# Kernel tuning notes

Measured on AMD Instinct MI355X. Metric: run time of the kernel, lower is better.

The kernel has to match this reference:

```python
import jax, jax.numpy as jnp
import numpy as np

ALPHA = 16
M_FACTORS = [8, 16, 8]
N_FACTORS = [8, 16, 8]


def setup_inputs() -> dict:
    key = jax.random.key(0)
    ks = jax.random.split(key, 9)
    B, S, D = 8, 2048, 1024
    r = 8
    x = jax.random.normal(ks[0], (B, S, D), dtype=jnp.float32)
    W = jax.random.normal(ks[1], (D, D), dtype=jnp.float32) * 0.02
    b = jax.random.normal(ks[2], (D,), dtype=jnp.float32) * 0.02
    # m-cores: (r_prev, m_i, r_next), first rank = 1
    core0 = jax.random.normal(ks[3], (1, 8, r), dtype=jnp.float32) * 0.1
    core1 = jax.random.normal(ks[4], (r, 16, r), dtype=jnp.float32) * 0.1
    core2 = jax.random.normal(ks[5], (r, 8, r), dtype=jnp.float32) * 0.1
    # n-cores: (r_prev, n_i, r_next), last rank = 1
    core3 = jax.random.normal(ks[6], (r, 8, r), dtype=jnp.float32) * 0.1
    core4 = jax.random.normal(ks[7], (r, 16, r), dtype=jnp.float32) * 0.1
    core5 = jax.random.normal(ks[8], (r, 8, 1), dtype=jnp.float32) * 0.1
    return {"x": x, "W": W, "b": b, "core0": core0, "core1": core1,
            "core2": core2, "core3": core3, "core4": core4, "core5": core5}


def tensorized_multiplication(x, m_cores, n_cores, m_factors):
    B, S, _ = x.shape
    # [B, 1, S, m_k, ..., m_1] : input dim split into m_factors, reversed
    tt = x.reshape((B, S) + tuple(m_factors[::-1]))[:, None]
    for core in m_cores:
        # contract trailing m-factor and current rank, new rank at axis 1
        tt = jnp.einsum('br...m,rmp->bp...', tt, core)
    for core in n_cores:
        # expand n-factor at the end, carry rank at axis 1
        tt = jnp.einsum('br...,rnp->bp...n', tt, core)
    # tt: [B, 1, S, n_1, ..., n_k] -> [B, S, prod(n_factors)]
    return tt.reshape(B, S, -1)


def reference(x, W, b, core0, core1, core2, core3, core4, core5):
    z = tensorized_multiplication(x, [core0, core1, core2],
                                  [core3, core4, core5], M_FACTORS)
    base = jnp.einsum('bsd,od->bso', x, W) + b  # nn.Linear: x @ W.T + b
    return base + z * ALPHA
```

## Files before the change

kernel.cpp:

```cpp
#include <hip/hip_runtime.h>
#include <hip/hip_bf16.h>


#define D_DIM 1024
#define BS_ROWS 16384
#define ALPHA_F 16.0f
#define BM 128
#define BN 128

using bf16   = __bf16;
using bf16x8 = __attribute__((ext_vector_type(8))) __bf16;
using bf16x4 = __attribute__((ext_vector_type(4))) __bf16;
using f32x4  = __attribute__((ext_vector_type(4))) float;
using f32x16 = __attribute__((ext_vector_type(16))) float;

#define GPTR(p) (const __attribute__((address_space(1))) void*)(p)
#define SPTR(p) (__attribute__((address_space(3))) void*)(p)

__global__ __launch_bounds__(256) void make_mn_kernel(
    const float* __restrict__ c0, const float* __restrict__ c1,
    const float* __restrict__ c2, const float* __restrict__ c3,
    const float* __restrict__ c4, const float* __restrict__ c5,
    float* __restrict__ Mws, float* __restrict__ NTws)
{
    __shared__ float sh[128 * 9];
    const int tid = threadIdx.x;

    if (blockIdx.x < 32) {
        for (int e = tid; e < 1024; e += 256) {
            int p2 = e & 7, i2i1 = e >> 3;
            int i1 = i2i1 & 7, i2 = i2i1 >> 3;
            float s = 0.f;
            for (int p1 = 0; p1 < 8; ++p1)
                s += c0[i1 * 8 + p1] * c1[p1 * 128 + i2 * 8 + p2];
            sh[i2i1 * 9 + p2] = s;
        }
        __syncthreads();
        int e = blockIdx.x * 256 + tid;
        int p3 = e & 7, d = e >> 3;
        int i1 = d & 7, i2 = (d >> 3) & 15, i3 = d >> 7;
        float s = 0.f;
        for (int p2 = 0; p2 < 8; ++p2)
            s += sh[(i2 * 8 + i1) * 9 + p2] * c2[p2 * 64 + i3 * 8 + p3];
        Mws[e] = s;
    } else {
        for (int e = tid; e < 1024; e += 256) {
            int p4 = e & 7, nn = e >> 3;
            int n2 = nn >> 3, n3 = nn & 7;
            float s = 0.f;
            for (int p5 = 0; p5 < 8; ++p5)
                s += c4[p4 * 128 + n2 * 8 + p5] * c5[p5 * 8 + n3];
            sh[nn * 9 + p4] = s;
        }
        __syncthreads();
        int e = (blockIdx.x - 32) * 256 + tid;
        int r3 = e & 7, o = e >> 3;
        int n1 = o >> 7, nn = o & 127;
        float s = 0.f;
        for (int p4 = 0; p4 < 8; ++p4)
            s += c3[r3 * 64 + n1 * 8 + p4] * sh[nn * 9 + p4];
        NTws[o * 8 + r3] = s;
    }
}

__global__ __launch_bounds__(256) void weff_cast_kernel(
    const float* __restrict__ X, const float* __restrict__ W,
    const float* __restrict__ Mws, const float* __restrict__ NTws,
    bf16* __restrict__ Weff, bf16* __restrict__ Xb)
{
    const int tid = threadIdx.x;
    if (blockIdx.x >= 512) {
        size_t i = ((size_t)(blockIdx.x - 512) * 256 + tid) * 8;
        f32x4 a = *(const f32x4*)&X[i];
        f32x4 b = *(const f32x4*)&X[i + 4];
        bf16x8 v;
        v[0] = (bf16)a[0]; v[1] = (bf16)a[1]; v[2] = (bf16)a[2]; v[3] = (bf16)a[3];
        v[4] = (bf16)b[0]; v[5] = (bf16)b[1]; v[6] = (bf16)b[2]; v[7] = (bf16)b[3];
        *(bf16x8*)&Xb[i] = v;
        return;
    }
    int e  = blockIdx.x * 256 + tid;
    int o  = e >> 7;
    int d0 = (e & 127) * 8;
    f32x4 nt0 = *(const f32x4*)&NTws[o * 8];
    f32x4 nt1 = *(const f32x4*)&NTws[o * 8 + 4];
    f32x4 w0 = *(const f32x4*)&W[(size_t)o * D_DIM + d0];
    f32x4 w1 = *(const f32x4*)&W[(size_t)o * D_DIM + d0 + 4];
    bf16x8 res;
    for (int k = 0; k < 8; ++k) {
        f32x4 m0 = *(const f32x4*)&Mws[(d0 + k) * 8];
        f32x4 m1 = *(const f32x4*)&Mws[(d0 + k) * 8 + 4];
        float acc = m0[0]*nt0[0] + m0[1]*nt0[1] + m0[2]*nt0[2] + m0[3]*nt0[3]
                  + m1[0]*nt1[0] + m1[1]*nt1[1] + m1[2]*nt1[2] + m1[3]*nt1[3];
        float w = (k < 4) ? w0[k] : w1[k - 4];
        res[k] = (bf16)(w + ALPHA_F * acc);
    }
    *(bf16x8*)&Weff[(size_t)o * D_DIM + d0] = res;
}

#define TBM 256
#define TBN 256
#define TBK 64
#define ABYT (TBM * TBK * 2)
#define BBYT (TBN * TBK * 2)
#define BUF4 (ABYT + BBYT)
#define NT4  (D_DIM / TBK)

__global__ __launch_bounds__(512, 2) void gemm_pipe4_kernel(
    const bf16* __restrict__ Xb,
    const bf16* __restrict__ Weff,
    const float* __restrict__ bias,
    float* __restrict__ Out)
{
    extern __shared__ __attribute__((aligned(16))) char smem[];

    const int tid  = threadIdx.x;
    const int wave = tid >> 6, lane = tid & 63;

    const int bid   = blockIdx.x;
    const int slot  = (bid & 7) * 32 + (bid >> 3);
    const int mtile = slot >> 2;
    const int ntile = slot & 3;

    const int wr = wave >> 2, wc = wave & 3;
    const int l31 = lane & 31, half = lane >> 5;
    const int rsw = l31 & 7;

    const int srow   = wave * 32 + (lane >> 3);
    const int gchunk = (lane & 7) ^ (lane >> 3);
    const bf16* asrc = Xb   + (size_t)(mtile * TBM + srow) * D_DIM + gchunk * 8;
    const bf16* bsrc = Weff + (size_t)(ntile * TBN + srow) * D_DIM + gchunk * 8;
    const int woff = wave * 4096;

    auto STAGE = [&](int bo, int t) {
        const bf16* ap = asrc + t * TBK;
        const bf16* bp = bsrc + t * TBK;
#pragma unroll
        for (int j = 0; j < 4; ++j)
            __builtin_amdgcn_global_load_lds(GPTR(ap + (size_t)j * 8 * D_DIM),
                                             SPTR(smem + bo + woff + j * 1024), 16, 0, 0);
#pragma unroll
        for (int j = 0; j < 4; ++j)
            __builtin_amdgcn_global_load_lds(GPTR(bp + (size_t)j * 8 * D_DIM),
                                             SPTR(smem + bo + ABYT + woff + j * 1024), 16, 0, 0);
    };

    f32x16 acc[4][2];
#pragma unroll
    for (int i = 0; i < 4; ++i)
#pragma unroll
        for (int j = 0; j < 2; ++j)
#pragma unroll
            for (int r = 0; r < 16; ++r) acc[i][j][r] = 0.f;

    auto COMPUTE = [&](int bo) {
        const char* Ab = smem + bo;
        const char* Bb = smem + bo + ABYT;
#pragma unroll
        for (int kk = 0; kk < 4; ++kk) {
            const int sb = (((kk * 2 + half) ^ rsw) * 16);
            bf16x8 af[4], bfr[2];
#pragma unroll
            for (int i = 0; i < 4; ++i)
                af[i] = *(const bf16x8*)(Ab + (wr * 128 + i * 32 + l31) * 128 + sb);
#pragma unroll
            for (int j = 0; j < 2; ++j)
                bfr[j] = *(const bf16x8*)(Bb + (wc * 64 + j * 32 + l31) * 128 + sb);
            __builtin_amdgcn_s_setprio(1);
#pragma unroll
            for (int i = 0; i < 4; ++i)
#pragma unroll
                for (int j = 0; j < 2; ++j)
                    acc[i][j] = __builtin_amdgcn_mfma_f32_32x32x16_bf16(
                        af[i], bfr[j], acc[i][j], 0, 0, 0);
            __builtin_amdgcn_s_setprio(0);
        }
    };

    STAGE(0, 0);
    STAGE(BUF4, 1);
    asm volatile("s_waitcnt vmcnt(8)" ::: "memory");
    __builtin_amdgcn_s_barrier();
    __builtin_amdgcn_sched_barrier(0);

    for (int t = 0; t < NT4 - 2; ++t) {
        const int bo = (t & 1) * BUF4;
        COMPUTE(bo);
        asm volatile("s_waitcnt lgkmcnt(0)" ::: "memory");
        __builtin_amdgcn_s_barrier();
        __builtin_amdgcn_sched_barrier(0);
        STAGE(bo, t + 2);
        asm volatile("s_waitcnt vmcnt(8)" ::: "memory");
        __builtin_amdgcn_s_barrier();
        __builtin_amdgcn_sched_barrier(0);
    }
    COMPUTE(((NT4 - 2) & 1) * BUF4);
    asm volatile("s_waitcnt lgkmcnt(0)" ::: "memory");
    __builtin_amdgcn_s_barrier();
    __builtin_amdgcn_sched_barrier(0);
    asm volatile("s_waitcnt vmcnt(0)" ::: "memory");
    __builtin_amdgcn_s_barrier();
    __builtin_amdgcn_sched_barrier(0);
    COMPUTE(((NT4 - 1) & 1) * BUF4);

    float bj[2];
#pragma unroll
    for (int j = 0; j < 2; ++j)
        bj[j] = bias[ntile * TBN + wc * 64 + j * 32 + l31];
#pragma unroll
    for (int i = 0; i < 4; ++i) {
        int rbase = mtile * TBM + wr * 128 + i * 32 + 4 * half;
#pragma unroll
        for (int j = 0; j < 2; ++j) {
            int col = ntile * TBN + wc * 64 + j * 32 + l31;
#pragma unroll
            for (int r = 0; r < 16; ++r) {
                int row = rbase + (r & 3) + 8 * (r >> 2);
                Out[(size_t)row * D_DIM + col] = acc[i][j][r] + bj[j];
            }
        }
    }
}

__global__ __launch_bounds__(256) void gemm_bb_kernel(
    const bf16* __restrict__ Xb,
    const bf16* __restrict__ Weff,
    const float* __restrict__ bias,
    float* __restrict__ Out)
{
    __shared__ __align__(16) bf16 As[BM][64];
    __shared__ __align__(16) bf16 Bs[BN][64];

    const int tid  = threadIdx.x;
    const int wave = tid >> 6, lane = tid & 63;
    const int mtile = blockIdx.x, ntile = blockIdx.y;
    const int wr = wave >> 1, wc = wave & 1;
    const int l15 = lane & 15, quad = lane >> 4;

    const int srow = wave * 32 + (lane >> 3);
    const int gchunk = (lane & 7) ^ (lane >> 3);
    const bf16* asrc = Xb   + (size_t)(mtile * BM + srow) * D_DIM + gchunk * 8;
    const bf16* bsrc = Weff + (size_t)(ntile * BN + srow) * D_DIM + gchunk * 8;
    char* abase = (char*)&As[0][0] + wave * 4096;
    char* bbase = (char*)&Bs[0][0] + wave * 4096;

    const int rsw = l15 & 7;

    f32x4 acc[4][4];
    for (int i = 0; i < 4; ++i)
        for (int j = 0; j < 4; ++j)
            for (int r = 0; r < 4; ++r) acc[i][j][r] = 0.f;

    for (int kt = 0; kt < D_DIM / 64; ++kt) {
        const int ko = kt * 64;
        for (int j = 0; j < 4; ++j) {
            __builtin_amdgcn_global_load_lds(GPTR(asrc + (size_t)j * 8 * D_DIM + ko),
                                             SPTR(abase + j * 1024), 16, 0, 0);
            __builtin_amdgcn_global_load_lds(GPTR(bsrc + (size_t)j * 8 * D_DIM + ko),
                                             SPTR(bbase + j * 1024), 16, 0, 0);
        }
        __syncthreads();
        for (int kk = 0; kk < 2; ++kk) {
            const int lc = kk * 4 + quad;
            const int sc = (lc ^ rsw) * 8;
            bf16x8 af[4], bfr[4];
            for (int i = 0; i < 4; ++i)
                af[i] = *(const bf16x8*)&As[wr * 64 + i * 16 + l15][sc];
            for (int j = 0; j < 4; ++j)
                bfr[j] = *(const bf16x8*)&Bs[wc * 64 + j * 16 + l15][sc];
            for (int i = 0; i < 4; ++i)
                for (int j = 0; j < 4; ++j)
                    acc[i][j] = __builtin_amdgcn_mfma_f32_16x16x32_bf16(
                        af[i], bfr[j], acc[i][j], 0, 0, 0);
        }
        __syncthreads();
    }

    float bj[4];
    for (int j = 0; j < 4; ++j)
        bj[j] = bias[ntile * BN + wc * 64 + j * 16 + l15];
    for (int i = 0; i < 4; ++i) {
        int row0 = mtile * BM + wr * 64 + i * 16 + quad * 4;
        for (int r = 0; r < 4; ++r) {
            float* orow = Out + (size_t)(row0 + r) * D_DIM + ntile * BN + wc * 64 + l15;
            for (int j = 0; j < 4; ++j)
                orow[j * 16] = acc[i][j][r] + bj[j];
        }
    }
}

__global__ __launch_bounds__(256) void gemm_bias_kernel(
    const float* __restrict__ X,
    const bf16* __restrict__ Weff,
    const float* __restrict__ bias,
    float* __restrict__ Out)
{
    __shared__ __align__(16) bf16 As[BM][32];
    __shared__ __align__(16) bf16 Bs[BN][32];

    const int tid  = threadIdx.x;
    const int wave = tid >> 6, lane = tid & 63;
    const int mtile = blockIdx.x, ntile = blockIdx.y;
    const int wr = wave >> 1, wc = wave & 1;
    const int l15 = lane & 15, quad = lane >> 4;

    const int ar = tid >> 1, ah = tid & 1;
    const float* xsrc = X + (size_t)(mtile * BM + ar) * D_DIM + ah * 16;
    bf16* adst = &As[ar][ah * 16];

    const bf16* bsrc0 = Weff + (size_t)(ntile * BN + wave * 32 + (lane >> 2)) * D_DIM
                        + (lane & 3) * 8;
    const bf16* bsrc1 = bsrc0 + 16 * D_DIM;
    char* bbase = (char*)&Bs[0][0];
    void* bdst0 = bbase + wave * 2048;
    void* bdst1 = bbase + wave * 2048 + 1024;

    f32x4 acc[4][4];
    for (int i = 0; i < 4; ++i)
        for (int j = 0; j < 4; ++j)
            for (int r = 0; r < 4; ++r) acc[i][j][r] = 0.f;

    for (int kt = 0; kt < D_DIM / 32; ++kt) {
        __builtin_amdgcn_global_load_lds(GPTR(bsrc0 + kt * 32), SPTR(bdst0), 16, 0, 0);
        __builtin_amdgcn_global_load_lds(GPTR(bsrc1 + kt * 32), SPTR(bdst1), 16, 0, 0);

        const f32x4* xp = (const f32x4*)(xsrc + kt * 32);
        f32x4 f0 = xp[0], f1 = xp[1], f2 = xp[2], f3 = xp[3];
        bf16x8 p0, p1;
        p0[0] = (bf16)f0[0]; p0[1] = (bf16)f0[1]; p0[2] = (bf16)f0[2]; p0[3] = (bf16)f0[3];
        p0[4] = (bf16)f1[0]; p0[5] = (bf16)f1[1]; p0[6] = (bf16)f1[2]; p0[7] = (bf16)f1[3];
        p1[0] = (bf16)f2[0]; p1[1] = (bf16)f2[1]; p1[2] = (bf16)f2[2]; p1[3] = (bf16)f2[3];
        p1[4] = (bf16)f3[0]; p1[5] = (bf16)f3[1]; p1[6] = (bf16)f3[2]; p1[7] = (bf16)f3[3];
        *(bf16x8*)adst = p0;
        *(bf16x8*)(adst + 8) = p1;

        __syncthreads();

        bf16x8 af[4], bfr[4];
        for (int i = 0; i < 4; ++i)
            af[i] = *(const bf16x8*)&As[wr * 64 + i * 16 + l15][quad * 8];
        for (int j = 0; j < 4; ++j)
            bfr[j] = *(const bf16x8*)&Bs[wc * 64 + j * 16 + l15][quad * 8];
        for (int i = 0; i < 4; ++i)
            for (int j = 0; j < 4; ++j)
                acc[i][j] = __builtin_amdgcn_mfma_f32_16x16x32_bf16(
                    af[i], bfr[j], acc[i][j], 0, 0, 0);

        __syncthreads();
    }

    float bj[4];
    for (int j = 0; j < 4; ++j)
        bj[j] = bias[ntile * BN + wc * 64 + j * 16 + l15];
    for (int i = 0; i < 4; ++i) {
        int row0 = mtile * BM + wr * 64 + i * 16 + quad * 4;
        for (int r = 0; r < 4; ++r) {
            float* orow = Out + (size_t)(row0 + r) * D_DIM + ntile * BN + wc * 64 + l15;
            for (int j = 0; j < 4; ++j)
                orow[j * 16] = acc[i][j][r] + bj[j];
        }
    }
}

__global__ __launch_bounds__(256) void build_weff_fused_kernel(
    const float* __restrict__ W,
    const float* __restrict__ c0, const float* __restrict__ c1,
    const float* __restrict__ c2, const float* __restrict__ c3,
    const float* __restrict__ c4, const float* __restrict__ c5,
    bf16* __restrict__ Weff)
{
    __shared__ float t2[1024];
    __shared__ float Msh[8192];
    const int tid = threadIdx.x;
    const int o = blockIdx.x;

    for (int e = tid; e < 1024; e += 256) {
        int p2 = e & 7, i2i1 = e >> 3;
        int i1 = i2i1 & 7, i2 = i2i1 >> 3;
        float s = 0.f;
        for (int p1 = 0; p1 < 8; ++p1)
            s += c0[i1 * 8 + p1] * c1[p1 * 128 + i2 * 8 + p2];
        t2[e] = s;
    }
    __syncthreads();
    for (int e = tid; e < 8192; e += 256) {
        int p3 = e & 7, d = e >> 3;
        int i1 = d & 7, i2 = (d >> 3) & 15, i3 = d >> 7;
        float s = 0.f;
        for (int p2 = 0; p2 < 8; ++p2)
            s += t2[(i2 * 8 + i1) * 8 + p2] * c2[p2 * 64 + i3 * 8 + p3];
        Msh[e] = s;
    }
    int n1 = o >> 7, nn = o & 127, n2 = nn >> 3, n3 = nn & 7;
    float v[8];
    for (int p4 = 0; p4 < 8; ++p4) {
        float s = 0.f;
        for (int p5 = 0; p5 < 8; ++p5)
            s += c4[p4 * 128 + n2 * 8 + p5] * c5[p5 * 8 + n3];
        v[p4] = s;
    }
    float ncol[8];
    for (int r3 = 0; r3 < 8; ++r3) {
        float s = 0.f;
        for (int p4 = 0; p4 < 8; ++p4)
            s += c3[r3 * 64 + n1 * 8 + p4] * v[p4];
        ncol[r3] = s;
    }
    __syncthreads();

    int d0 = tid * 4;
    f32x4 w = *(const f32x4*)&W[o * D_DIM + d0];
    bf16x4 res;
    for (int k = 0; k < 4; ++k) {
        float acc = 0.f;
        for (int r = 0; r < 8; ++r)
            acc += Msh[(d0 + k) * 8 + r] * ncol[r];
        res[k] = (bf16)(w[k] + ALPHA_F * acc);
    }
    *(bf16x4*)&Weff[o * D_DIM + d0] = res;
}

extern "C" void kernel_launch(void* const* d_in, const int* in_sizes, int n_in,
                              void* d_out, int out_size, void* d_ws, size_t ws_size,
                              hipStream_t stream) {
    const float* x  = (const float*)d_in[0];
    const float* W  = (const float*)d_in[1];
    const float* b  = (const float*)d_in[2];
    const float* c0 = (const float*)d_in[3];
    const float* c1 = (const float*)d_in[4];
    const float* c2 = (const float*)d_in[5];
    const float* c3 = (const float*)d_in[6];
    const float* c4 = (const float*)d_in[7];
    const float* c5 = (const float*)d_in[8];
    float* out = (float*)d_out;

    char* ws = (char*)d_ws;
    bf16*  Weff = (bf16*)ws;
    float* Mws  = (float*)(ws + 2u * 1024u * 1024u);
    float* NTws = Mws + 8192;
    bf16*  Xb   = (bf16*)(ws + 4u * 1024u * 1024u);
    const size_t need = 4u * 1024u * 1024u + (size_t)BS_ROWS * D_DIM * 2u;

    static int smem_ok = -1;
    if (smem_ok < 0) {
        hipError_t e = hipFuncSetAttribute((const void*)gemm_pipe4_kernel,
                                           hipFuncAttributeMaxDynamicSharedMemorySize,
                                           2 * BUF4);
        smem_ok = (e == hipSuccess) ? 1 : 0;
    }

    if (ws_size >= need) {
        make_mn_kernel<<<64, 256, 0, stream>>>(c0, c1, c2, c3, c4, c5, Mws, NTws);
        weff_cast_kernel<<<512 + 8192, 256, 0, stream>>>(x, W, Mws, NTws, Weff, Xb);
        if (smem_ok) {
            gemm_pipe4_kernel<<<dim3(256), 512, 2 * BUF4, stream>>>(Xb, Weff, b, out);
        } else {
            dim3 grid(BS_ROWS / BM, D_DIM / BN);
            gemm_bb_kernel<<<grid, 256, 0, stream>>>(Xb, Weff, b, out);
        }
    } else {
        build_weff_fused_kernel<<<D_DIM, 256, 0, stream>>>(W, c0, c1, c2, c3, c4, c5, Weff);
        dim3 grid(BS_ROWS / BM, D_DIM / BN);
        gemm_bias_kernel<<<grid, 256, 0, stream>>>(x, Weff, b, out);
    }
}
```

Before: 163.9 us.

## Switch GEMM to 16x16x32 MFMA tiles with simplified double-buffer pipeline

Replaces the 32x32x16 MFMA tiling with 16x16x32 bf16 MFMAs, giving each wave an 8x4 grid of 16x16 accumulators and streaming A fragments one at a time. The prefetch schedule also changes: it now issues the next stage before computing the current one and waits on vmcnt(0) every iteration, instead of the earlier two-stage-ahead schedule with partial vmcnt waits. The goal is better MFMA issue and a simpler pipeline with coalesced output stores. The risk is that the full vmcnt(0) wait each iteration exposes load latency, and the smaller MFMAs need more LDS fragment reads.

```diff
diff --git a/kernel.cpp b/kernel.cpp
--- a/kernel.cpp
+++ b/kernel.cpp
@@ -12,7 +12,6 @@
 using bf16x8 = __attribute__((ext_vector_type(8))) __bf16;
 using bf16x4 = __attribute__((ext_vector_type(4))) __bf16;
 using f32x4  = __attribute__((ext_vector_type(4))) float;
-using f32x16 = __attribute__((ext_vector_type(16))) float;
 
 #define GPTR(p) (const __attribute__((address_space(1))) void*)(p)
 #define SPTR(p) (__attribute__((address_space(3))) void*)(p)
@@ -103,10 +102,10 @@
 #define TBK 64
 #define ABYT (TBM * TBK * 2)
 #define BBYT (TBN * TBK * 2)
-#define BUF4 (ABYT + BBYT)
-#define NT4  (D_DIM / TBK)
-
-__global__ __launch_bounds__(512, 2) void gemm_pipe4_kernel(
+#define BUF5 (ABYT + BBYT)
+#define NT5  (D_DIM / TBK)
+
+__global__ __launch_bounds__(512, 2) void gemm_pipe5_kernel(
     const bf16* __restrict__ Xb,
     const bf16* __restrict__ Weff,
     const float* __restrict__ bias,
@@ -123,8 +122,8 @@
     const int ntile = slot & 3;
 
     const int wr = wave >> 2, wc = wave & 3;
-    const int l31 = lane & 31, half = lane >> 5;
-    const int rsw = l31 & 7;
+    const int l15 = lane & 15, quad = lane >> 4;
+    const int rsw = l15 & 7;
 
     const int srow   = wave * 32 + (lane >> 3);
     const int gchunk = (lane & 7) ^ (lane >> 3);
@@ -145,79 +144,66 @@
                                              SPTR(smem + bo + ABYT + woff + j * 1024), 16, 0, 0);
     };
 
-    f32x16 acc[4][2];
-#pragma unroll
-    for (int i = 0; i < 4; ++i)
-#pragma unroll
-        for (int j = 0; j < 2; ++j)
-#pragma unroll
-            for (int r = 0; r < 16; ++r) acc[i][j][r] = 0.f;
+    f32x4 acc[8][4];
+#pragma unroll
+    for (int i = 0; i < 8; ++i)
+#pragma unroll
+        for (int j = 0; j < 4; ++j)
+#pragma unroll
+            for (int r = 0; r < 4; ++r) acc[i][j][r] = 0.f;
 
     auto COMPUTE = [&](int bo) {
         const char* Ab = smem + bo;
         const char* Bb = smem + bo + ABYT;
 #pragma unroll
-        for (int kk = 0; kk < 4; ++kk) {
-            const int sb = (((kk * 2 + half) ^ rsw) * 16);
-            bf16x8 af[4], bfr[2];
-#pragma unroll
-            for (int i = 0; i < 4; ++i)
-                af[i] = *(const bf16x8*)(Ab + (wr * 128 + i * 32 + l31) * 128 + sb);
-#pragma unroll
-            for (int j = 0; j < 2; ++j)
-                bfr[j] = *(const bf16x8*)(Bb + (wc * 64 + j * 32 + l31) * 128 + sb);
-            __builtin_amdgcn_s_setprio(1);
-#pragma unroll
-            for (int i = 0; i < 4; ++i)
-#pragma unroll
-                for (int j = 0; j < 2; ++j)
-                    acc[i][j] = __builtin_amdgcn_mfma_f32_32x32x16_bf16(
-                        af[i], bfr[j], acc[i][j], 0, 0, 0);
-            __builtin_amdgcn_s_setprio(0);
+        for (int kk = 0; kk < 2; ++kk) {
+            const int sb = ((kk * 4 + quad) ^ rsw) * 16;
+            bf16x8 bfr[4];
+#pragma unroll
+            for (int j = 0; j < 4; ++j)
+                bfr[j] = *(const bf16x8*)(Bb + (wc * 64 + j * 16 + l15) * 128 + sb);
+#pragma unroll
+            for (int i = 0; i < 8; ++i) {
+                bf16x8 af = *(const bf16x8*)(Ab + (wr * 128 + i * 16 + l15) * 128 + sb);
+                __builtin_amdgcn_s_setprio(1);
+#pragma unroll
+                for (int j = 0; j < 4; ++j)
+                    acc[i][j] = __builtin_amdgcn_mfma_f32_16x16x32_bf16(
+                        af, bfr[j], acc[i][j], 0, 0, 0);
+                __builtin_amdgcn_s_setprio(0);
+            }
         }
     };
 
     STAGE(0, 0);
-    STAGE(BUF4, 1);
-    asm volatile("s_waitcnt vmcnt(8)" ::: "memory");
-    __builtin_amdgcn_s_barrier();
-    __builtin_amdgcn_sched_barrier(0);
-
-    for (int t = 0; t < NT4 - 2; ++t) {
-        const int bo = (t & 1) * BUF4;
-        COMPUTE(bo);
-        asm volatile("s_waitcnt lgkmcnt(0)" ::: "memory");
-        __builtin_amdgcn_s_barrier();
-        __builtin_amdgcn_sched_barrier(0);
-        STAGE(bo, t + 2);
-        asm volatile("s_waitcnt vmcnt(8)" ::: "memory");
-        __builtin_amdgcn_s_barrier();
-        __builtin_amdgcn_sched_barrier(0);
-    }
-    COMPUTE(((NT4 - 2) & 1) * BUF4);
-    asm volatile("s_waitcnt lgkmcnt(0)" ::: "memory");
-    __builtin_amdgcn_s_barrier();
-    __builtin_amdgcn_sched_barrier(0);
     asm volatile("s_waitcnt vmcnt(0)" ::: "memory");
     __builtin_amdgcn_s_barrier();
     __builtin_amdgcn_sched_barrier(0);
-    COMPUTE(((NT4 - 1) & 1) * BUF4);
-
-    float bj[2];
-#pragma unroll
-    for (int j = 0; j < 2; ++j)
-        bj[j] = bias[ntile * TBN + wc * 64 + j * 32 + l31];
-#pragma unroll
-    for (int i = 0; i < 4; ++i) {
-        int rbase = mtile * TBM + wr * 128 + i * 32 + 4 * half;
-#pragma unroll
-        for (int j = 0; j < 2; ++j) {
-            int col = ntile * TBN + wc * 64 + j * 32 + l31;
-#pragma unroll
-            for (int r = 0; r < 16; ++r) {
-                int row = rbase + (r & 3) + 8 * (r >> 2);
-                Out[(size_t)row * D_DIM + col] = acc[i][j][r] + bj[j];
-            }
+
+    int cur = 0;
+    for (int t = 0; t < NT5 - 1; ++t) {
+        STAGE((cur ^ 1) * BUF5, t + 1);
+        COMPUTE(cur * BUF5);
+        asm volatile("s_waitcnt vmcnt(0) lgkmcnt(0)" ::: "memory");
+        __builtin_amdgcn_s_barrier();
+        __builtin_amdgcn_sched_barrier(0);
+        cur ^= 1;
+    }
+    COMPUTE(cur * BUF5);
+
+    float bj[4];
+#pragma unroll
+    for (int j = 0; j < 4; ++j)
+        bj[j] = bias[ntile * TBN + wc * 64 + j * 16 + l15];
+#pragma unroll
+    for (int i = 0; i < 8; ++i) {
+        int row0 = mtile * TBM + wr * 128 + i * 16 + quad * 4;
+#pragma unroll
+        for (int r = 0; r < 4; ++r) {
+            float* orow = Out + (size_t)(row0 + r) * D_DIM + ntile * TBN + wc * 64 + l15;
+#pragma unroll
+            for (int j = 0; j < 4; ++j)
+                orow[j * 16] = acc[i][j][r] + bj[j];
         }
     }
 }
@@ -443,9 +429,9 @@
 
     static int smem_ok = -1;
     if (smem_ok < 0) {
-        hipError_t e = hipFuncSetAttribute((const void*)gemm_pipe4_kernel,
+        hipError_t e = hipFuncSetAttribute((const void*)gemm_pipe5_kernel,
                                            hipFuncAttributeMaxDynamicSharedMemorySize,
-                                           2 * BUF4);
+                                           2 * BUF5);
         smem_ok = (e == hipSuccess) ? 1 : 0;
     }
 
@@ -453,7 +439,7 @@
         make_mn_kernel<<<64, 256, 0, stream>>>(c0, c1, c2, c3, c4, c5, Mws, NTws);
         weff_cast_kernel<<<512 + 8192, 256, 0, stream>>>(x, W, Mws, NTws, Weff, Xb);
         if (smem_ok) {
-            gemm_pipe4_kernel<<<dim3(256), 512, 2 * BUF4, stream>>>(Xb, Weff, b, out);
+            gemm_pipe5_kernel<<<dim3(256), 512, 2 * BUF5, stream>>>(Xb, Weff, b, out);
         } else {
             dim3 grid(BS_ROWS / BM, D_DIM / BN);
             gemm_bb_kernel<<<grid, 256, 0, stream>>>(Xb, Weff, b, out);
```

Measured after the change: 164.9 us. About the same (+0.6%).
